# Kernel optimization log

Measured on AMD Instinct MI355X. Metric: run time of the kernel, lower is better.

## Reference

```python
import jax, jax.numpy as jnp
import numpy as np

NEG_SLOPE = 0.2

def _leaky_relu(x):
    return jnp.where(x >= 0, x, NEG_SLOPE * x)

def setup_inputs() -> dict:
    key = jax.random.key(0)
    ks = jax.random.split(key, 12)
    B, N, M = 64, 4096, 128
    d_ope, d_ma, d_out = 6, 3, 8
    return {
        "ope_ma_adj": jax.random.randint(ks[0], (B, N, M), 0, 2, dtype=jnp.int32),
        "batch_idxes": jnp.arange(B, dtype=jnp.int32),
        "ope_feat": jax.random.normal(ks[1], (B, N, d_ope), dtype=jnp.float32),
        "ma_feat": jax.random.normal(ks[2], (B, M, d_ma), dtype=jnp.float32),
        "proc_time": jax.random.uniform(ks[3], (B, N, M), dtype=jnp.float32),
        "W_src": jax.random.normal(ks[4], (d_ope, d_out), dtype=jnp.float32),
        "W_dst": jax.random.normal(ks[5], (d_ma, d_out), dtype=jnp.float32),
        "w_edge": jax.random.normal(ks[6], (d_out,), dtype=jnp.float32),
        "attn_l": jax.random.normal(ks[7], (d_out,), dtype=jnp.float32),
        "attn_r": jax.random.normal(ks[8], (d_out,), dtype=jnp.float32),
        "attn_e": jax.random.normal(ks[9], (d_out,), dtype=jnp.float32),
    }

def reference(ope_ma_adj, batch_idxes, ope_feat, ma_feat, proc_time,
              W_src, W_dst, w_edge, attn_l, attn_r, attn_e):
    # GATedge.forward with num_head=1 (head dim folded away).
    adj_i = ope_ma_adj[batch_idxes]            # [B,N,M] int (0/1)
    adj = adj_i.astype(jnp.float32)
    feat_src = ope_feat @ W_src                # [B,N,d]
    feat_dst = ma_feat @ W_dst                 # [B,M,d]
    el = feat_src @ attn_l                     # [B,N]
    er = feat_dst @ attn_r                     # [B,M]
    # fc_edge is Linear(1,d): feat_edge = proc[...,None]*w_edge, so
    # ee = (feat_edge*attn_e).sum(-1) = proc * dot(w_edge, attn_e)
    ee = proc_time * jnp.dot(w_edge, attn_e)   # [B,N,M]
    a = adj * el[:, :, None] + ee + adj * er[:, None, :]
    eijk = _leaky_relu(a)                      # [B,N,M]
    ekk = _leaky_relu(2.0 * er)                # [B,M]
    neg_inf = jnp.asarray(-jnp.inf, dtype=eijk.dtype)
    eijk_m = jnp.where(adj_i == 1, eijk, neg_inf)
    e = jnp.concatenate([eijk_m, ekk[:, None, :]], axis=1)   # [B,N+1,M]
    alpha = jax.nn.softmax(e, axis=1)          # softmax over ops (+self)
    alpha_ijk = alpha[:, :-1, :]               # [B,N,M]
    alpha_kk = alpha[:, -1, :]                 # [B,M]
    # b = sum_j alpha_ijk * (feat_edge + feat_src), split to avoid [B,N,M,d]
    b_edge = jnp.einsum('bnm,bnm->bm', alpha_ijk, proc_time)[..., None] * w_edge  # [B,M,d]
    b_src = jnp.einsum('bnm,bnd->bmd', alpha_ijk, feat_src)                       # [B,M,d]
    c = feat_dst * alpha_kk[..., None]         # [B,M,d]
    return jax.nn.sigmoid(b_edge + b_src + c)  # nu_k_prime [B,M,d]
```

## Files before the change

### kernel.cpp

```cpp
#include <hip/hip_runtime.h>
#include <hip/hip_bf16.h>

constexpr int B  = 64;
constexpr int N  = 4096;
constexpr int M  = 128;
constexpr int DO = 8;
constexpr int NC = 32;
constexpr int CH = N / NC;
constexpr float CEXP = 20.0f;

__global__ __launch_bounds__(128) void hgnn_k1(
    const int*   __restrict__ adj,
    const int*   __restrict__ bidx,
    const float* __restrict__ ope_feat,
    const float* __restrict__ ma_feat,
    const float* __restrict__ proc,
    const float* __restrict__ W_src,
    const float* __restrict__ W_dst,
    const float* __restrict__ w_edge,
    const float* __restrict__ attn_l,
    const float* __restrict__ attn_r,
    const float* __restrict__ attn_e,
    float*       __restrict__ part)
{
    const int chunk = blockIdx.x;
    const int b     = blockIdx.y;
    const int m     = threadIdx.x;
    const int n0    = chunk * CH;

    __shared__ __align__(16) float fs[CH][DO];
    __shared__ float el_s[CH];

    float er = 0.f;
    {
        const float* mf = ma_feat + ((size_t)b * M + m) * 3;
        const float f0 = mf[0], f1 = mf[1], f2 = mf[2];
#pragma unroll
        for (int d = 0; d < DO; ++d) {
            const float fd = f0 * W_dst[d] + f1 * W_dst[DO + d] + f2 * W_dst[2 * DO + d];
            er += fd * attn_r[d];
        }
    }
    float cee = 0.f;
#pragma unroll
    for (int d = 0; d < DO; ++d) cee += w_edge[d] * attn_e[d];

    {
        const int r = threadIdx.x;
        const float* of = ope_feat + ((size_t)b * N + (n0 + r)) * 6;
        const float o0 = of[0], o1 = of[1], o2 = of[2], o3 = of[3], o4 = of[4], o5 = of[5];
        float el = 0.f;
#pragma unroll
        for (int d = 0; d < DO; ++d) {
            const float f = o0 * W_src[d] + o1 * W_src[DO + d] + o2 * W_src[2 * DO + d] +
                            o3 * W_src[3 * DO + d] + o4 * W_src[4 * DO + d] + o5 * W_src[5 * DO + d];
            fs[r][d] = f;
            el += f * attn_l[d];
        }
        el_s[r] = el;
    }
    __syncthreads();

    const int ab = bidx[b];
    const int*   ap = adj  + ((size_t)ab * N + n0) * M + m;
    const float* pp = proc + ((size_t)b  * N + n0) * M + m;

    float l = 0.f, sp = 0.f;
    float sf[DO];
#pragma unroll
    for (int d = 0; d < DO; ++d) sf[d] = 0.f;

    auto step = [&](int a, float p, int r) {
        float v = el_s[r] + er + cee * p;
        v = (v >= 0.f) ? v : 0.2f * v;
        const float vm = (a != 0) ? v : -1e30f;
        const float w  = __expf(vm - CEXP);
        l += w;
        sp = fmaf(w, p, sp);
        const float4 f0 = *reinterpret_cast<const float4*>(&fs[r][0]);
        const float4 f1 = *reinterpret_cast<const float4*>(&fs[r][4]);
        sf[0] = fmaf(w, f0.x, sf[0]);
        sf[1] = fmaf(w, f0.y, sf[1]);
        sf[2] = fmaf(w, f0.z, sf[2]);
        sf[3] = fmaf(w, f0.w, sf[3]);
        sf[4] = fmaf(w, f1.x, sf[4]);
        sf[5] = fmaf(w, f1.y, sf[5]);
        sf[6] = fmaf(w, f1.z, sf[6]);
        sf[7] = fmaf(w, f1.w, sf[7]);
    };

    for (int r = 0; r < CH; r += 4) {
        const int   a0 = ap[(size_t)(r + 0) * M];
        const int   a1 = ap[(size_t)(r + 1) * M];
        const int   a2 = ap[(size_t)(r + 2) * M];
        const int   a3 = ap[(size_t)(r + 3) * M];
        const float p0 = pp[(size_t)(r + 0) * M];
        const float p1 = pp[(size_t)(r + 1) * M];
        const float p2 = pp[(size_t)(r + 2) * M];
        const float p3 = pp[(size_t)(r + 3) * M];
        step(a0, p0, r + 0);
        step(a1, p1, r + 1);
        step(a2, p2, r + 2);
        step(a3, p3, r + 3);
    }

    const size_t base   = ((size_t)b * NC + chunk) * M + m;
    const size_t stride = (size_t)B * NC * M;
    part[base]          = l;
    part[stride + base] = sp;
#pragma unroll
    for (int d = 0; d < DO; ++d) part[(2 + d) * stride + base] = sf[d];
}

__global__ __launch_bounds__(256) void hgnn_k2(
    const float* __restrict__ ma_feat,
    const float* __restrict__ W_dst,
    const float* __restrict__ w_edge,
    const float* __restrict__ attn_r,
    const float* __restrict__ part,
    float*       __restrict__ out)
{
    const int t = blockIdx.x * 256 + threadIdx.x;
    if (t >= B * M) return;
    const int m = t & (M - 1);
    const int b = t >> 7;

    const size_t stride = (size_t)B * NC * M;

    float acc[10];
#pragma unroll
    for (int f = 0; f < 10; ++f) acc[f] = 0.f;

    for (int c = 0; c < NC; c += 4) {
        float tmp[4][10];
#pragma unroll
        for (int j = 0; j < 4; ++j) {
            const size_t base = ((size_t)b * NC + (c + j)) * M + m;
#pragma unroll
            for (int f = 0; f < 10; ++f) tmp[j][f] = part[(size_t)f * stride + base];
        }
#pragma unroll
        for (int j = 0; j < 4; ++j)
#pragma unroll
            for (int f = 0; f < 10; ++f) acc[f] += tmp[j][f];
    }

    const float* mf = ma_feat + ((size_t)b * M + m) * 3;
    const float f0 = mf[0], f1 = mf[1], f2 = mf[2];
    float fd[DO];
    float er = 0.f;
#pragma unroll
    for (int d = 0; d < DO; ++d) {
        fd[d] = f0 * W_dst[d] + f1 * W_dst[DO + d] + f2 * W_dst[2 * DO + d];
        er += fd[d] * attn_r[d];
    }
    float ekk = 2.f * er;
    ekk = (ekk >= 0.f) ? ekk : 0.2f * ekk;
    const float wkk = __expf(ekk - CEXP);

    const float L    = acc[0] + wkk;
    const float invL = 1.f / L;
    const float akk  = wkk * invL;
    const float spf  = acc[1] * invL;

#pragma unroll
    for (int d = 0; d < DO; ++d) {
        const float x = spf * w_edge[d] + acc[2 + d] * invL + fd[d] * akk;
        out[(size_t)t * DO + d] = 1.f / (1.f + __expf(-x));
    }
}

extern "C" void kernel_launch(void* const* d_in, const int* in_sizes, int n_in,
                              void* d_out, int out_size, void* d_ws, size_t ws_size,
                              hipStream_t stream) {
    const int*   adj      = (const int*)  d_in[0];
    const int*   bidx     = (const int*)  d_in[1];
    const float* ope_feat = (const float*)d_in[2];
    const float* ma_feat  = (const float*)d_in[3];
    const float* proc     = (const float*)d_in[4];
    const float* W_src    = (const float*)d_in[5];
    const float* W_dst    = (const float*)d_in[6];
    const float* w_edge   = (const float*)d_in[7];
    const float* attn_l   = (const float*)d_in[8];
    const float* attn_r   = (const float*)d_in[9];
    const float* attn_e   = (const float*)d_in[10];
    float* out  = (float*)d_out;
    float* part = (float*)d_ws;

    hgnn_k1<<<dim3(NC, B), 128, 0, stream>>>(adj, bidx, ope_feat, ma_feat, proc,
                                             W_src, W_dst, w_edge, attn_l, attn_r,
                                             attn_e, part);
    hgnn_k2<<<dim3((B * M + 255) / 256), 256, 0, stream>>>(ma_feat, W_dst, w_edge,
                                                           attn_r, part, out);
}
```

Measured before the change: 306.4 us.

## Vectorize adjacency/proc loads with 4 columns per thread and cross-wave reduction

Remaps the first kernel so each thread covers four consecutive machine columns, loading them as int4/float4, and four sub-groups of 32 threads split the chunk's rows. Partial sums are combined with a cross-half-wave shuffle plus a shared-memory step, then written as float4 stores. The goal is fewer, wider global loads and less per-element instruction overhead in a bandwidth-bound streaming loop. In exchange there are 40 live accumulators per thread, a second block barrier, and a launch-bounds occupancy hint that adds register pressure.

```diff
diff --git a/kernel.cpp b/kernel.cpp
--- a/kernel.cpp
+++ b/kernel.cpp
@@ -9,7 +9,7 @@
 constexpr int CH = N / NC;
 constexpr float CEXP = 20.0f;
 
-__global__ __launch_bounds__(128) void hgnn_k1(
+__global__ __launch_bounds__(128, 4) void hgnn_k1(
     const int*   __restrict__ adj,
     const int*   __restrict__ bidx,
     const float* __restrict__ ope_feat,
@@ -25,91 +25,131 @@
 {
     const int chunk = blockIdx.x;
     const int b     = blockIdx.y;
-    const int m     = threadIdx.x;
+    const int t     = threadIdx.x;
+    const int sub   = t >> 5;
+    const int mq    = t & 31;
+    const int m0    = mq * 4;
     const int n0    = chunk * CH;
 
     __shared__ __align__(16) float fs[CH][DO];
     __shared__ float el_s[CH];
-
-    float er = 0.f;
-    {
-        const float* mf = ma_feat + ((size_t)b * M + m) * 3;
+    __shared__ float red[32][41];
+
+    float er4[4];
+#pragma unroll
+    for (int c = 0; c < 4; ++c) {
+        const float* mf = ma_feat + ((size_t)b * M + (m0 + c)) * 3;
         const float f0 = mf[0], f1 = mf[1], f2 = mf[2];
+        float er = 0.f;
 #pragma unroll
         for (int d = 0; d < DO; ++d) {
             const float fd = f0 * W_dst[d] + f1 * W_dst[DO + d] + f2 * W_dst[2 * DO + d];
             er += fd * attn_r[d];
         }
+        er4[c] = er;
     }
     float cee = 0.f;
 #pragma unroll
     for (int d = 0; d < DO; ++d) cee += w_edge[d] * attn_e[d];
 
     {
-        const int r = threadIdx.x;
-        const float* of = ope_feat + ((size_t)b * N + (n0 + r)) * 6;
+        const float* of = ope_feat + ((size_t)b * N + (n0 + t)) * 6;
         const float o0 = of[0], o1 = of[1], o2 = of[2], o3 = of[3], o4 = of[4], o5 = of[5];
         float el = 0.f;
 #pragma unroll
         for (int d = 0; d < DO; ++d) {
             const float f = o0 * W_src[d] + o1 * W_src[DO + d] + o2 * W_src[2 * DO + d] +
                             o3 * W_src[3 * DO + d] + o4 * W_src[4 * DO + d] + o5 * W_src[5 * DO + d];
-            fs[r][d] = f;
+            fs[t][d] = f;
             el += f * attn_l[d];
         }
-        el_s[r] = el;
+        el_s[t] = el;
     }
     __syncthreads();
 
     const int ab = bidx[b];
-    const int*   ap = adj  + ((size_t)ab * N + n0) * M + m;
-    const float* pp = proc + ((size_t)b  * N + n0) * M + m;
-
-    float l = 0.f, sp = 0.f;
-    float sf[DO];
-#pragma unroll
-    for (int d = 0; d < DO; ++d) sf[d] = 0.f;
-
-    auto step = [&](int a, float p, int r) {
-        float v = el_s[r] + er + cee * p;
-        v = (v >= 0.f) ? v : 0.2f * v;
-        const float vm = (a != 0) ? v : -1e30f;
-        const float w  = __expf(vm - CEXP);
-        l += w;
-        sp = fmaf(w, p, sp);
-        const float4 f0 = *reinterpret_cast<const float4*>(&fs[r][0]);
-        const float4 f1 = *reinterpret_cast<const float4*>(&fs[r][4]);
-        sf[0] = fmaf(w, f0.x, sf[0]);
-        sf[1] = fmaf(w, f0.y, sf[1]);
-        sf[2] = fmaf(w, f0.z, sf[2]);
-        sf[3] = fmaf(w, f0.w, sf[3]);
-        sf[4] = fmaf(w, f1.x, sf[4]);
-        sf[5] = fmaf(w, f1.y, sf[5]);
-        sf[6] = fmaf(w, f1.z, sf[6]);
-        sf[7] = fmaf(w, f1.w, sf[7]);
-    };
-
-    for (int r = 0; r < CH; r += 4) {
-        const int   a0 = ap[(size_t)(r + 0) * M];
-        const int   a1 = ap[(size_t)(r + 1) * M];
-        const int   a2 = ap[(size_t)(r + 2) * M];
-        const int   a3 = ap[(size_t)(r + 3) * M];
-        const float p0 = pp[(size_t)(r + 0) * M];
-        const float p1 = pp[(size_t)(r + 1) * M];
-        const float p2 = pp[(size_t)(r + 2) * M];
-        const float p3 = pp[(size_t)(r + 3) * M];
-        step(a0, p0, r + 0);
-        step(a1, p1, r + 1);
-        step(a2, p2, r + 2);
-        step(a3, p3, r + 3);
-    }
-
-    const size_t base   = ((size_t)b * NC + chunk) * M + m;
-    const size_t stride = (size_t)B * NC * M;
-    part[base]          = l;
-    part[stride + base] = sp;
-#pragma unroll
-    for (int d = 0; d < DO; ++d) part[(2 + d) * stride + base] = sf[d];
+    const int*   ap = adj  + ((size_t)ab * N + (n0 + sub)) * M + m0;
+    const float* pp = proc + ((size_t)b  * N + (n0 + sub)) * M + m0;
+
+    float l4[4]  = {0.f, 0.f, 0.f, 0.f};
+    float sp4[4] = {0.f, 0.f, 0.f, 0.f};
+    float sf4[4][DO];
+#pragma unroll
+    for (int c = 0; c < 4; ++c)
+#pragma unroll
+        for (int d = 0; d < DO; ++d) sf4[c][d] = 0.f;
+
+    for (int j = 0; j < 32; j += 4) {
+        int4   A[4];
+        float4 P[4];
+#pragma unroll
+        for (int u = 0; u < 4; ++u) {
+            const size_t off = (size_t)(4 * (j + u)) * M;
+            A[u] = *reinterpret_cast<const int4*>(ap + off);
+            P[u] = *reinterpret_cast<const float4*>(pp + off);
+        }
+#pragma unroll
+        for (int u = 0; u < 4; ++u) {
+            const int r = 4 * (j + u) + sub;
+            const float  el = el_s[r];
+            const float4 f0 = *reinterpret_cast<const float4*>(&fs[r][0]);
+            const float4 f1 = *reinterpret_cast<const float4*>(&fs[r][4]);
+            const int   av[4] = {A[u].x, A[u].y, A[u].z, A[u].w};
+            const float pv[4] = {P[u].x, P[u].y, P[u].z, P[u].w};
+#pragma unroll
+            for (int c = 0; c < 4; ++c) {
+                float v = el + er4[c] + cee * pv[c];
+                v = (v >= 0.f) ? v : 0.2f * v;
+                const float vm = (av[c] != 0) ? v : -1e30f;
+                const float w  = __expf(vm - CEXP);
+                l4[c] += w;
+                sp4[c] = fmaf(w, pv[c], sp4[c]);
+                sf4[c][0] = fmaf(w, f0.x, sf4[c][0]);
+                sf4[c][1] = fmaf(w, f0.y, sf4[c][1]);
+                sf4[c][2] = fmaf(w, f0.z, sf4[c][2]);
+                sf4[c][3] = fmaf(w, f0.w, sf4[c][3]);
+                sf4[c][4] = fmaf(w, f1.x, sf4[c][4]);
+                sf4[c][5] = fmaf(w, f1.y, sf4[c][5]);
+                sf4[c][6] = fmaf(w, f1.z, sf4[c][6]);
+                sf4[c][7] = fmaf(w, f1.w, sf4[c][7]);
+            }
+        }
+    }
+
+    float v[40];
+#pragma unroll
+    for (int c = 0; c < 4; ++c) { v[c] = l4[c]; v[4 + c] = sp4[c]; }
+#pragma unroll
+    for (int c = 0; c < 4; ++c)
+#pragma unroll
+        for (int d = 0; d < DO; ++d) v[8 + c * DO + d] = sf4[c][d];
+
+#pragma unroll
+    for (int f = 0; f < 40; ++f) v[f] += __shfl_down(v[f], 32);
+
+    if (t >= 64 && t < 96) {
+#pragma unroll
+        for (int f = 0; f < 40; ++f) red[mq][f] = v[f];
+    }
+    __syncthreads();
+
+    if (t < 32) {
+#pragma unroll
+        for (int f = 0; f < 40; ++f) v[f] += red[t][f];
+
+        const size_t stride  = (size_t)B * NC * M;
+        const size_t rowbase = ((size_t)b * NC + chunk) * M;
+        float4* p0 = reinterpret_cast<float4*>(part + rowbase);
+        p0[(0 * stride) / 4 * 0 + t] = make_float4(v[0], v[1], v[2], v[3]);
+        reinterpret_cast<float4*>(part + stride + rowbase)[t] =
+            make_float4(v[4], v[5], v[6], v[7]);
+#pragma unroll
+        for (int d = 0; d < DO; ++d) {
+            reinterpret_cast<float4*>(part + (size_t)(2 + d) * stride + rowbase)[t] =
+                make_float4(v[8 + 0 * DO + d], v[8 + 1 * DO + d],
+                            v[8 + 2 * DO + d], v[8 + 3 * DO + d]);
+        }
+    }
 }
 
 __global__ __launch_bounds__(256) void hgnn_k2(
```

Measured after the change: 307.5 us. Within noise of the previous version (+0.4%).

## Double-buffer adjacency/proc tiles via async global-to-LDS loads with 256 threads

Applied to the files above, without the earlier changes.

Rewrites the main streaming loop of the first kernel so that 8-row tiles of the adjacency and proc_time arrays are copied asynchronously into double-buffered shared memory using global_load_lds. The next tile is prefetched while the current one is consumed. The block grows to 256 threads, with two halves each handling 4 rows per tile, and their partial sums are combined through shared memory at the end. The goal is to hide memory latency and raise the number of loads in flight on this bandwidth-bound kernel. In exchange it adds two barriers per tile (64 tiles per block) and uses more shared memory.

```diff
diff --git a/kernel.cpp b/kernel.cpp
--- a/kernel.cpp
+++ b/kernel.cpp
@@ -7,9 +7,14 @@
 constexpr int DO = 8;
 constexpr int NC = 32;
 constexpr int CH = N / NC;
+constexpr int TR = 8;
+constexpr int NT = CH / TR;
 constexpr float CEXP = 20.0f;
 
-__global__ __launch_bounds__(128) void hgnn_k1(
+typedef __attribute__((address_space(3))) void       lds_void;
+typedef const __attribute__((address_space(1))) void gbl_void;
+
+__global__ __launch_bounds__(256) void hgnn_k1(
     const int*   __restrict__ adj,
     const int*   __restrict__ bidx,
     const float* __restrict__ ope_feat,
@@ -25,11 +30,31 @@
 {
     const int chunk = blockIdx.x;
     const int b     = blockIdx.y;
-    const int m     = threadIdx.x;
+    const int t     = threadIdx.x;
+    const int m     = t & 127;
+    const int sub   = t >> 7;
+    const int w     = t >> 6;
     const int n0    = chunk * CH;
 
+    __shared__ __align__(16) int   bufA[2][TR * M];
+    __shared__ __align__(16) float bufP[2][TR * M];
     __shared__ __align__(16) float fs[CH][DO];
     __shared__ float el_s[CH];
+    __shared__ float red[M][12];
+
+    const int ab = bidx[b];
+
+    const int elemoff = w * 256 + (t & 63) * 4;
+    auto issue_tile = [&](int j, int pq) {
+        const int* gA = adj  + ((size_t)ab * N + n0 + (size_t)j * TR) * M + elemoff;
+        const float* gP = proc + ((size_t)b * N + n0 + (size_t)j * TR) * M + elemoff;
+        __builtin_amdgcn_global_load_lds((gbl_void*)gA,
+                                         (lds_void*)&bufA[pq][w * 256], 16, 0, 0);
+        __builtin_amdgcn_global_load_lds((gbl_void*)gP,
+                                         (lds_void*)&bufP[pq][w * 256], 16, 0, 0);
+    };
+
+    issue_tile(0, 0);
 
     float er = 0.f;
     {
@@ -45,71 +70,78 @@
 #pragma unroll
     for (int d = 0; d < DO; ++d) cee += w_edge[d] * attn_e[d];
 
-    {
-        const int r = threadIdx.x;
-        const float* of = ope_feat + ((size_t)b * N + (n0 + r)) * 6;
+    if (t < CH) {
+        const float* of = ope_feat + ((size_t)b * N + (n0 + t)) * 6;
         const float o0 = of[0], o1 = of[1], o2 = of[2], o3 = of[3], o4 = of[4], o5 = of[5];
         float el = 0.f;
 #pragma unroll
         for (int d = 0; d < DO; ++d) {
             const float f = o0 * W_src[d] + o1 * W_src[DO + d] + o2 * W_src[2 * DO + d] +
                             o3 * W_src[3 * DO + d] + o4 * W_src[4 * DO + d] + o5 * W_src[5 * DO + d];
-            fs[r][d] = f;
+            fs[t][d] = f;
             el += f * attn_l[d];
         }
-        el_s[r] = el;
-    }
-    __syncthreads();
-
-    const int ab = bidx[b];
-    const int*   ap = adj  + ((size_t)ab * N + n0) * M + m;
-    const float* pp = proc + ((size_t)b  * N + n0) * M + m;
+        el_s[t] = el;
+    }
 
     float l = 0.f, sp = 0.f;
     float sf[DO];
 #pragma unroll
     for (int d = 0; d < DO; ++d) sf[d] = 0.f;
 
-    auto step = [&](int a, float p, int r) {
-        float v = el_s[r] + er + cee * p;
-        v = (v >= 0.f) ? v : 0.2f * v;
-        const float vm = (a != 0) ? v : -1e30f;
-        const float w  = __expf(vm - CEXP);
-        l += w;
-        sp = fmaf(w, p, sp);
-        const float4 f0 = *reinterpret_cast<const float4*>(&fs[r][0]);
-        const float4 f1 = *reinterpret_cast<const float4*>(&fs[r][4]);
-        sf[0] = fmaf(w, f0.x, sf[0]);
-        sf[1] = fmaf(w, f0.y, sf[1]);
-        sf[2] = fmaf(w, f0.z, sf[2]);
-        sf[3] = fmaf(w, f0.w, sf[3]);
-        sf[4] = fmaf(w, f1.x, sf[4]);
-        sf[5] = fmaf(w, f1.y, sf[5]);
-        sf[6] = fmaf(w, f1.z, sf[6]);
-        sf[7] = fmaf(w, f1.w, sf[7]);
-    };
-
-    for (int r = 0; r < CH; r += 4) {
-        const int   a0 = ap[(size_t)(r + 0) * M];
-        const int   a1 = ap[(size_t)(r + 1) * M];
-        const int   a2 = ap[(size_t)(r + 2) * M];
-        const int   a3 = ap[(size_t)(r + 3) * M];
-        const float p0 = pp[(size_t)(r + 0) * M];
-        const float p1 = pp[(size_t)(r + 1) * M];
-        const float p2 = pp[(size_t)(r + 2) * M];
-        const float p3 = pp[(size_t)(r + 3) * M];
-        step(a0, p0, r + 0);
-        step(a1, p1, r + 1);
-        step(a2, p2, r + 2);
-        step(a3, p3, r + 3);
-    }
-
-    const size_t base   = ((size_t)b * NC + chunk) * M + m;
-    const size_t stride = (size_t)B * NC * M;
-    part[base]          = l;
-    part[stride + base] = sp;
-#pragma unroll
-    for (int d = 0; d < DO; ++d) part[(2 + d) * stride + base] = sf[d];
+    for (int j = 0; j < NT; ++j) {
+        __syncthreads();
+        if (j + 1 < NT) issue_tile(j + 1, (j + 1) & 1);
+        __syncthreads();
+
+        const int pq = j & 1;
+#pragma unroll
+        for (int k = 0; k < 4; ++k) {
+            const int lr = sub * 4 + k;
+            const int r  = j * TR + lr;
+            const int   a = bufA[pq][lr * M + m];
+            const float p = bufP[pq][lr * M + m];
+            const float el = el_s[r];
+            const float4 f0 = *reinterpret_cast<const float4*>(&fs[r][0]);
+            const float4 f1 = *reinterpret_cast<const float4*>(&fs[r][4]);
+
+            float v = el + er + cee * p;
+            v = (v >= 0.f) ? v : 0.2f * v;
+            const float vm = (a != 0) ? v : -1e30f;
+            const float wt = __expf(vm - CEXP);
+            l += wt;
+            sp = fmaf(wt, p, sp);
+            sf[0] = fmaf(wt, f0.x, sf[0]);
+            sf[1] = fmaf(wt, f0.y, sf[1]);
+            sf[2] = fmaf(wt, f0.z, sf[2]);
+            sf[3] = fmaf(wt, f0.w, sf[3]);
+            sf[4] = fmaf(wt, f1.x, sf[4]);
+            sf[5] = fmaf(wt, f1.y, sf[5]);
+            sf[6] = fmaf(wt, f1.z, sf[6]);
+            sf[7] = fmaf(wt, f1.w, sf[7]);
+        }
+    }
+
+    if (sub == 1) {
+        red[m][0] = l;
+        red[m][1] = sp;
+#pragma unroll
+        for (int d = 0; d < DO; ++d) red[m][2 + d] = sf[d];
+    }
+    __syncthreads();
+    if (sub == 0) {
+        l  += red[m][0];
+        sp += red[m][1];
+#pragma unroll
+        for (int d = 0; d < DO; ++d) sf[d] += red[m][2 + d];
+
+        const size_t stride = (size_t)B * NC * M;
+        const size_t base   = ((size_t)b * NC + chunk) * M + m;
+        part[base]          = l;
+        part[stride + base] = sp;
+#pragma unroll
+        for (int d = 0; d < DO; ++d) part[(size_t)(2 + d) * stride + base] = sf[d];
+    }
 }
 
 __global__ __launch_bounds__(256) void hgnn_k2(
@@ -187,7 +219,7 @@
     float* out  = (float*)d_out;
     float* part = (float*)d_ws;
 
-    hgnn_k1<<<dim3(NC, B), 128, 0, stream>>>(adj, bidx, ope_feat, ma_feat, proc,
+    hgnn_k1<<<dim3(NC, B), 256, 0, stream>>>(adj, bidx, ope_feat, ma_feat, proc,
                                              W_src, W_dst, w_edge, attn_l, attn_r,
                                              attn_e, part);
     hgnn_k2<<<dim3((B * M + 255) / 256), 256, 0, stream>>>(ma_feat, W_dst, w_edge,
```

After: 309.4 us. Within noise of the previous version (+1.0%).
